# Kernel optimization log

Hardware: AMD Instinct MI355X
Metric: run time of the kernel (lower is better)

## Reference

```python
import jax, jax.numpy as jnp
import numpy as np
from jax import lax

N, D, H, O = 16384, 512, 1024, 512
G, E, K = 3, 4, 2
ALPHA = 0.01


def setup_inputs() -> dict:
    key = jax.random.key(0)
    ks = jax.random.split(key, 16)

    def lin(k, out_d, in_d):
        s = 1.0 / np.sqrt(in_d)
        return jax.random.uniform(k, (out_d, in_d), jnp.float32, -s, s)

    x = jax.random.normal(ks[0], (N, D), jnp.float32)
    Wm = lin(ks[1], G, D)
    bm = jnp.zeros((G,), jnp.float32)
    # group routers stacked: [G, E, D]
    Wr = jax.random.uniform(ks[2], (G, E, D), jnp.float32, -1 / np.sqrt(D), 1 / np.sqrt(D))
    br = jnp.zeros((G, E), jnp.float32)
    # expert params stacked over (group, expert)
    W1 = jax.random.uniform(ks[3], (G, E, H, D), jnp.float32, -1 / np.sqrt(D), 1 / np.sqrt(D))
    b1 = jnp.zeros((G, E, H), jnp.float32)
    W2 = jax.random.uniform(ks[4], (G, E, H, H), jnp.float32, -1 / np.sqrt(H), 1 / np.sqrt(H))
    b2 = jnp.zeros((G, E, H), jnp.float32)
    Wp = jax.random.uniform(ks[5], (G, E, H, D), jnp.float32, -1 / np.sqrt(D), 1 / np.sqrt(D))
    bp = jnp.zeros((G, E, H), jnp.float32)
    W3 = jax.random.uniform(ks[6], (G, E, O, H), jnp.float32, -1 / np.sqrt(H), 1 / np.sqrt(H))
    b3 = jnp.zeros((G, E, O), jnp.float32)
    return {"x": x, "Wm": Wm, "bm": bm, "Wr": Wr, "br": br,
            "W1": W1, "b1": b1, "W2": W2, "b2": b2,
            "Wp": Wp, "bp": bp, "W3": W3, "b3": b3}


def _expert(x, W1, b1, W2, b2, Wp, bp, W3, b3):
    # residual MLP (dropout in eval mode => identity)
    h = jax.nn.relu(x @ W1.T + b1)
    h = h @ W2.T + b2
    ident = x @ Wp.T + bp  # projection (input_dim != hidden_dim)
    h = jax.nn.relu(h + ident)
    return h @ W3.T + b3


def reference(x, Wm, bm, Wr, br, W1, b1, W2, b2, Wp, bp, W3, b3):
    n = x.shape[0]
    # ---- meta (top-1 group) routing ----
    meta_logits = x @ Wm.T + bm                         # [N, G]
    g = jnp.argmax(meta_logits, axis=1)                 # top-1 group per token
    pm = jax.nn.softmax(meta_logits, axis=1).mean(0)    # [G]
    aux = ALPHA * G * jnp.sum(pm * pm)
    # ---- per-group router logits, gathered for each token's group ----
    logits_all = jnp.einsum('nd,ged->nge', x, Wr) + br  # [N, G, E]
    sel = jnp.take_along_axis(logits_all, g[:, None, None], axis=1)[:, 0, :]  # [N, E]
    # ---- group-level load-balancing aux loss (over tokens in each group) ----
    probs = jax.nn.softmax(sel, axis=-1)                # [N, E]
    onehot_g = (g[:, None] == jnp.arange(G)[None, :])   # [N, G] bool
    cnt = onehot_g.sum(0)                               # [G]
    mean_g = (onehot_g.astype(x.dtype).T @ probs) / jnp.maximum(cnt, 1)[:, None].astype(x.dtype)
    aux = aux + jnp.sum(jnp.where(cnt > 0, ALPHA * E * jnp.sum(mean_g * mean_g, -1), 0.0))
    # ---- top-k expert weights within selected group (softmax over the k logits) ----
    vals, idx = lax.top_k(sel, K)                       # [N, K]
    w = jax.nn.softmax(vals, axis=-1)                   # [N, K]
    cw = jnp.zeros((n, E), x.dtype).at[jnp.arange(n)[:, None], idx].set(w)   # [N, E]
    combine = cw[:, None, :] * onehot_g[:, :, None].astype(x.dtype)          # [N, G, E]
    # ---- expert compute + combine (loop over the fixed small set of experts) ----
    out = jnp.zeros((n, O), x.dtype)
    for gi in range(G):
        for e in range(E):
            y = _expert(x, W1[gi, e], b1[gi, e], W2[gi, e], b2[gi, e],
                        Wp[gi, e], bp[gi, e], W3[gi, e], b3[gi, e])
            out = out + combine[:, gi, e:e + 1] * y
    return out, aux
```

## Files before the change

kernel.cpp:

```cpp
#include <hip/hip_runtime.h>
#include <hip/hip_bf16.h>

#define N_TOK 16384
#define DDIM  512
#define HDIM  1024
#define ODIM  512
#define NG    3
#define NE    4
#define NGE   12
#define TASK_CAP 272

typedef __bf16 bf16x8 __attribute__((ext_vector_type(8)));
typedef float  f32x4  __attribute__((ext_vector_type(4)));
typedef unsigned int u32;

__device__ __forceinline__ void gld_lds16(const void* gsrc, void* ldst) {
    __builtin_amdgcn_global_load_lds(
        (const __attribute__((address_space(1))) u32*)gsrc,
        (__attribute__((address_space(3))) u32*)ldst, 16, 0, 0);
}

static constexpr size_t OFF_WSLOT = 512;
static constexpr size_t OFF_ELIST = OFF_WSLOT + (size_t)N_TOK*2*4;
static constexpr size_t OFF_TASK  = 917504;
static constexpr size_t OFF_XBF   = 1048576;
static constexpr size_t OFF_W1    = OFF_XBF + (size_t)N_TOK*DDIM*2;
static constexpr size_t OFF_W2    = OFF_W1  + (size_t)NGE*HDIM*DDIM*2;
static constexpr size_t OFF_WP    = OFF_W2  + (size_t)NGE*HDIM*HDIM*2;
static constexpr size_t OFF_W3    = OFF_WP  + (size_t)NGE*HDIM*DDIM*2;
static constexpr size_t OFF_H1    = OFF_W3  + (size_t)NGE*ODIM*HDIM*2;
static constexpr size_t OFF_U     = OFF_H1  + (size_t)N_TOK*2*HDIM*2;
static constexpr size_t OFF_Y     = OFF_U   + (size_t)N_TOK*2*HDIM*2;
static constexpr size_t WS_NEED   = OFF_Y   + (size_t)N_TOK*2*ODIM*2;

__global__ void cast_all_k(const float* __restrict__ x,  const float* __restrict__ w1,
                           const float* __restrict__ w2, const float* __restrict__ wp,
                           const float* __restrict__ w3,
                           __bf16* xbf, __bf16* w1b, __bf16* w2b, __bf16* wpb, __bf16* w3b) {
    int tid = blockIdx.x * blockDim.x + threadIdx.x;
    int stride = gridDim.x * blockDim.x;
    auto seg = [&](const float* __restrict__ s, __bf16* __restrict__ d, int n4) {
        const float4* s4 = (const float4*)s;
        uint2* d4 = (uint2*)d;
        for (int i = tid; i < n4; i += stride) {
            float4 v = s4[i];
            union { __bf16 h[4]; uint2 u; } o;
            o.h[0] = (__bf16)v.x; o.h[1] = (__bf16)v.y;
            o.h[2] = (__bf16)v.z; o.h[3] = (__bf16)v.w;
            d4[i] = o.u;
        }
    };
    seg(x,  xbf, N_TOK*DDIM/4);
    seg(w1, w1b, NGE*HDIM*DDIM/4);
    seg(w2, w2b, NGE*HDIM*HDIM/4);
    seg(wp, wpb, NGE*HDIM*DDIM/4);
    seg(w3, w3b, NGE*ODIM*HDIM/4);
}

__global__ __launch_bounds__(256) void routing_k(
        const float* __restrict__ x,  const float* __restrict__ Wm,
        const float* __restrict__ bm, const float* __restrict__ Wr,
        const float* __restrict__ br,
        float* pmsum, float* psum, int* cnt, int* ecount,
        int* elist, float* wslot) {
    __shared__ float lpm[NG];
    __shared__ float lpsum[NGE];
    __shared__ int   lcnt[NG];
    __shared__ int   lec[NGE];
    __shared__ int   lbase[NGE];
    __shared__ int   lentry[NGE][64];

    int tid = threadIdx.x;
    if (tid < NG)  { lpm[tid] = 0.f; lcnt[tid] = 0; }
    if (tid < NGE) { lpsum[tid] = 0.f; lec[tid] = 0; }
    __syncthreads();

    int wid = tid >> 6, lane = tid & 63;

    #pragma unroll 1
    for (int i = 0; i < 16; ++i) {
        int t = blockIdx.x * 64 + i * 4 + wid;

        const float4* xr = (const float4*)(x + (size_t)t * DDIM);
        float4 xa = xr[lane*2], xb = xr[lane*2+1];

        float meta[NG];
        #pragma unroll
        for (int gi = 0; gi < NG; ++gi) {
            const float4* w = (const float4*)(Wm + gi*DDIM);
            float4 wa = w[lane*2], wb = w[lane*2+1];
            float s = xa.x*wa.x + xa.y*wa.y + xa.z*wa.z + xa.w*wa.w
                    + xb.x*wb.x + xb.y*wb.y + xb.z*wb.z + xb.w*wb.w;
            #pragma unroll
            for (int off = 32; off > 0; off >>= 1) s += __shfl_xor(s, off);
            meta[gi] = s + bm[gi];
        }
        int g = 0;
        if (meta[1] > meta[g]) g = 1;
        if (meta[2] > meta[g]) g = 2;

        float mm = fmaxf(meta[0], fmaxf(meta[1], meta[2]));
        float e0 = expf(meta[0]-mm), e1 = expf(meta[1]-mm), e2 = expf(meta[2]-mm);
        float inv = 1.f / (e0 + e1 + e2);

        float sel[NE];
        #pragma unroll
        for (int e = 0; e < NE; ++e) {
            const float4* w = (const float4*)(Wr + (size_t)(g*NE + e)*DDIM);
            float4 wa = w[lane*2], wb = w[lane*2+1];
            float s = xa.x*wa.x + xa.y*wa.y + xa.z*wa.z + xa.w*wa.w
                    + xb.x*wb.x + xb.y*wb.y + xb.z*wb.z + xb.w*wb.w;
            #pragma unroll
            for (int off = 32; off > 0; off >>= 1) s += __shfl_xor(s, off);
            sel[e] = s + br[g*NE + e];
        }
        float ms = fmaxf(fmaxf(sel[0],sel[1]), fmaxf(sel[2],sel[3]));
        float pe[NE]; float ss = 0.f;
        #pragma unroll
        for (int e = 0; e < NE; ++e) { pe[e] = expf(sel[e]-ms); ss += pe[e]; }
        float invs = 1.f / ss;

        int i0 = 0;
        #pragma unroll
        for (int e = 1; e < NE; ++e) if (sel[e] > sel[i0]) i0 = e;
        int i1 = (i0 == 0) ? 1 : 0;
        #pragma unroll
        for (int e = 0; e < NE; ++e) if (e != i0 && sel[e] > sel[i1]) i1 = e;
        float ew = expf(sel[i1] - sel[i0]);
        float wden = 1.f / (1.f + ew);

        if (lane == 0) {
            atomicAdd(&lpm[0], e0*inv);
            atomicAdd(&lpm[1], e1*inv);
            atomicAdd(&lpm[2], e2*inv);
            #pragma unroll
            for (int e = 0; e < NE; ++e) atomicAdd(&lpsum[g*NE + e], pe[e]*invs);
            atomicAdd(&lcnt[g], 1);
            int ee0 = g*NE + i0, ee1 = g*NE + i1;
            int p0 = atomicAdd(&lec[ee0], 1);
            lentry[ee0][p0] = t*2;
            int p1 = atomicAdd(&lec[ee1], 1);
            lentry[ee1][p1] = t*2 + 1;
            wslot[t*2]   = wden;
            wslot[t*2+1] = ew * wden;
        }
    }
    __syncthreads();

    if (tid < NG)  { atomicAdd(pmsum + tid, lpm[tid]); atomicAdd(cnt + tid, lcnt[tid]); }
    if (tid < NGE) { atomicAdd(psum + tid, lpsum[tid]);
                     lbase[tid] = atomicAdd(ecount + tid, lec[tid]); }
    __syncthreads();

    for (int e = wid; e < NGE; e += 4) {
        int c = lec[e], base = lbase[e];
        for (int j = lane; j < c; j += 64)
            elist[e*N_TOK + base + j] = lentry[e][j];
    }
}

__global__ void finalize_aux_k(const float* pmsum, const float* psum, const int* cnt,
                               const int* ecount, int2* tasks, int* ntasks,
                               float* outAux) {
    if (threadIdx.x != 0 || blockIdx.x != 0) return;
    float s = 0.f;
    for (int i = 0; i < NG; ++i) { float p = pmsum[i] / (float)N_TOK; s += p*p; }
    float aux = 0.01f * NG * s;
    for (int gg = 0; gg < NG; ++gg) {
        int c = cnt[gg];
        if (c > 0) {
            float s2 = 0.f;
            for (int e = 0; e < NE; ++e) { float m = psum[gg*NE+e] / (float)c; s2 += m*m; }
            aux += 0.01f * NE * s2;
        }
    }
    *outAux = aux;
    int nt = 0;
    for (int ge = 0; ge < NGE; ++ge) {
        int c = ecount[ge];
        for (int m0 = 0; m0 < c; m0 += 128) tasks[nt++] = make_int2(ge, m0);
    }
    *ntasks = nt;
}

template<int NDIM, bool RELU, bool TWOPASS>
__global__ __launch_bounds__(256) void expert_gemm_k(
        const __bf16* __restrict__ A1, int shift1, int k1, const __bf16* __restrict__ B1,
        const __bf16* __restrict__ A2, int shift2, int k2, const __bf16* __restrict__ B2,
        const float* __restrict__ bias1, const float* __restrict__ bias2,
        __bf16* __restrict__ Out,
        const int* __restrict__ ecount, const int* __restrict__ elist,
        const int2* __restrict__ tasks, const int* __restrict__ ntasks) {
    if (blockIdx.y >= *ntasks) return;
    int2 tk = tasks[blockIdx.y];
    int ge = tk.x, m0 = tk.y;
    int cntE = ecount[ge];
    int n0 = blockIdx.x * 128;

    __shared__ __align__(16) char ldsA[2][16384];
    __shared__ __align__(16) char ldsB[2][16384];
    __shared__ int ents[128];

    int tid = threadIdx.x;
    if (tid < 128) {
        int r = m0 + tid;
        if (r >= cntE) r = cntE - 1;
        ents[tid] = elist[ge*N_TOK + r];
    }
    __syncthreads();

    int lane = tid & 63, wv = tid >> 6;
    int wm = wv >> 1, wn = wv & 1;
    int lr = lane & 15, lg = lane >> 4;
    int rl = lane >> 3;
    int csw = (lane & 7) ^ rl;
    int rsw = lr & 7;

    const char* sA1[4]; const char* sB1[4];
    const char* sA2[4]; const char* sB2[4];
    size_t rowB1 = (size_t)k1 * 2;
    const char* Bb1 = (const char*)(B1 + (size_t)ge * NDIM * k1) + (size_t)n0 * rowB1;
    #pragma unroll
    for (int j = 0; j < 4; ++j) {
        int r = wv*32 + j*8 + rl;
        sA1[j] = (const char*)A1 + (size_t)(ents[r] >> shift1) * rowB1 + (size_t)csw*16;
        sB1[j] = Bb1 + (size_t)r * rowB1 + (size_t)csw*16;
    }
    if constexpr (TWOPASS) {
        size_t rowB2 = (size_t)k2 * 2;
        const char* Bb2 = (const char*)(B2 + (size_t)ge * NDIM * k2) + (size_t)n0 * rowB2;
        #pragma unroll
        for (int j = 0; j < 4; ++j) {
            int r = wv*32 + j*8 + rl;
            sA2[j] = (const char*)A2 + (size_t)(ents[r] >> shift2) * rowB2 + (size_t)csw*16;
            sB2[j] = Bb2 + (size_t)r * rowB2 + (size_t)csw*16;
        }
    }

    int nk1 = k1 >> 6;
    int nk  = TWOPASS ? nk1 + (k2 >> 6) : nk1;

    auto stage = [&](int s) {
        int b = s & 1;
        if (!TWOPASS || s < nk1) {
            size_t ko = (size_t)s << 7;
            #pragma unroll
            for (int j = 0; j < 4; ++j) {
                gld_lds16(sA1[j] + ko, ldsA[b] + (wv*4 + j)*1024);
                gld_lds16(sB1[j] + ko, ldsB[b] + (wv*4 + j)*1024);
            }
        } else {
            size_t ko = (size_t)(s - nk1) << 7;
            #pragma unroll
            for (int j = 0; j < 4; ++j) {
                gld_lds16(sA2[j] + ko, ldsA[b] + (wv*4 + j)*1024);
                gld_lds16(sB2[j] + ko, ldsB[b] + (wv*4 + j)*1024);
            }
        }
    };

    f32x4 acc[4][4] = {};

    stage(0);
    __syncthreads();

    #pragma unroll 1
    for (int s = 0; s < nk; ++s) {
        if (s + 1 < nk) stage(s + 1);
        const char* bA = ldsA[s & 1];
        const char* bB = ldsB[s & 1];
        #pragma unroll
        for (int kk = 0; kk < 2; ++kk) {
            bf16x8 av[4], bv[4];
            #pragma unroll
            for (int mi = 0; mi < 4; ++mi) {
                int ar = wm*64 + mi*16 + lr;
                av[mi] = *(const bf16x8*)(bA + ar*128 + ((((kk*4+lg) ^ rsw)) << 4));
            }
            #pragma unroll
            for (int ni = 0; ni < 4; ++ni) {
                int br_ = wn*64 + ni*16 + lr;
                bv[ni] = *(const bf16x8*)(bB + br_*128 + ((((kk*4+lg) ^ rsw)) << 4));
            }
            #pragma unroll
            for (int mi = 0; mi < 4; ++mi)
                #pragma unroll
                for (int ni = 0; ni < 4; ++ni)
                    acc[mi][ni] = __builtin_amdgcn_mfma_f32_16x16x32_bf16(
                        av[mi], bv[ni], acc[mi][ni], 0, 0, 0);
        }
        __syncthreads();
    }

    #pragma unroll
    for (int ni = 0; ni < 4; ++ni) {
        int col = n0 + wn*64 + ni*16 + lr;
        float b = bias1[(size_t)ge*NDIM + col];
        if constexpr (TWOPASS) b += bias2[(size_t)ge*NDIM + col];
        #pragma unroll
        for (int mi = 0; mi < 4; ++mi) {
            #pragma unroll
            for (int j = 0; j < 4; ++j) {
                int rloc = wm*64 + mi*16 + lg*4 + j;
                if (m0 + rloc < cntE) {
                    float v = acc[mi][ni][j] + b;
                    if constexpr (RELU) v = fmaxf(v, 0.f);
                    Out[(size_t)ents[rloc] * NDIM + col] = (__bf16)v;
                }
            }
        }
    }
}

__global__ void combine_k(const __bf16* __restrict__ Y, const float* __restrict__ wslot,
                          float* __restrict__ out) {
    int idx = blockIdx.x * blockDim.x + threadIdx.x;
    int t = idx >> 6;
    int o = (idx & 63) * 8;
    bf16x8 y0 = *(const bf16x8*)(Y + (size_t)(2*t)   * ODIM + o);
    bf16x8 y1 = *(const bf16x8*)(Y + (size_t)(2*t+1) * ODIM + o);
    float w0 = wslot[2*t], w1 = wslot[2*t+1];
    float4 r0, r1;
    r0.x = w0*(float)y0[0] + w1*(float)y1[0];
    r0.y = w0*(float)y0[1] + w1*(float)y1[1];
    r0.z = w0*(float)y0[2] + w1*(float)y1[2];
    r0.w = w0*(float)y0[3] + w1*(float)y1[3];
    r1.x = w0*(float)y0[4] + w1*(float)y1[4];
    r1.y = w0*(float)y0[5] + w1*(float)y1[5];
    r1.z = w0*(float)y0[6] + w1*(float)y1[6];
    r1.w = w0*(float)y0[7] + w1*(float)y1[7];
    float* op = out + (size_t)t * ODIM + o;
    ((float4*)op)[0] = r0;
    ((float4*)op)[1] = r1;
}

extern "C" void kernel_launch(void* const* d_in, const int* in_sizes, int n_in,
                              void* d_out, int out_size, void* d_ws, size_t ws_size,
                              hipStream_t stream) {
    const float* x  = (const float*)d_in[0];
    const float* Wm = (const float*)d_in[1];
    const float* bm = (const float*)d_in[2];
    const float* Wr = (const float*)d_in[3];
    const float* br = (const float*)d_in[4];
    const float* W1 = (const float*)d_in[5];
    const float* b1 = (const float*)d_in[6];
    const float* W2 = (const float*)d_in[7];
    const float* b2 = (const float*)d_in[8];
    const float* Wp = (const float*)d_in[9];
    const float* bp = (const float*)d_in[10];
    const float* W3 = (const float*)d_in[11];
    const float* b3 = (const float*)d_in[12];

    if (ws_size < WS_NEED) return;

    char* ws = (char*)d_ws;
    float* outp = (float*)d_out;

    float* pmsum  = (float*)ws;
    float* psum   = (float*)ws + 4;
    int*   cnt    = (int*)ws + 16;
    int*   ecount = (int*)ws + 20;
    int*   ntasks = (int*)ws + 34;
    float* wslot  = (float*)(ws + OFF_WSLOT);
    int*   elist  = (int*)(ws + OFF_ELIST);
    int2*  tasks  = (int2*)(ws + OFF_TASK);
    __bf16* xbf = (__bf16*)(ws + OFF_XBF);
    __bf16* w1b = (__bf16*)(ws + OFF_W1);
    __bf16* w2b = (__bf16*)(ws + OFF_W2);
    __bf16* wpb = (__bf16*)(ws + OFF_WP);
    __bf16* w3b = (__bf16*)(ws + OFF_W3);
    __bf16* H1  = (__bf16*)(ws + OFF_H1);
    __bf16* U   = (__bf16*)(ws + OFF_U);
    __bf16* Y   = (__bf16*)(ws + OFF_Y);

    hipMemsetAsync(d_ws, 0, 512, stream);

    cast_all_k<<<4096, 256, 0, stream>>>(x, W1, W2, Wp, W3, xbf, w1b, w2b, wpb, w3b);

    routing_k<<<256, 256, 0, stream>>>(x, Wm, bm, Wr, br,
                                       pmsum, psum, cnt, ecount, elist, wslot);

    finalize_aux_k<<<1, 64, 0, stream>>>(pmsum, psum, cnt, ecount, tasks, ntasks,
                                         outp + (size_t)N_TOK*ODIM);

    dim3 gA(HDIM/128, TASK_CAP, 1);
    expert_gemm_k<HDIM, true, false><<<gA, 256, 0, stream>>>(
        xbf, 1, DDIM, w1b, nullptr, 0, 0, nullptr, b1, nullptr, H1,
        ecount, elist, tasks, ntasks);

    expert_gemm_k<HDIM, true, true><<<gA, 256, 0, stream>>>(
        H1, 0, HDIM, w2b, xbf, 1, DDIM, wpb, b2, bp, U,
        ecount, elist, tasks, ntasks);

    dim3 gC(ODIM/128, TASK_CAP, 1);
    expert_gemm_k<ODIM, false, false><<<gC, 256, 0, stream>>>(
        U, 0, HDIM, w3b, nullptr, 0, 0, nullptr, b3, nullptr, Y,
        ecount, elist, tasks, ntasks);

    combine_k<<<4096, 256, 0, stream>>>(Y, wslot, outp);
}
```

Baseline: 473.9 us.

## Fuse three expert GEMMs into one kernel keeping hidden activations in LDS

Replaces the three separate grouped expert GEMM launches with one fused kernel. Each 512-thread block processes a 64-token tile through W1, W2+Wp and W3, keeping the hidden activations in a 128KB LDS buffer instead of writing H1 and U to global memory. Tasks are remapped so consecutive tasks land on the same XCD. The cost is that weight operands are now read straight from global memory with no LDS staging or double buffering, occupancy is limited by the large LDS footprint, and only 64-row tiles with one block per tile are available for parallelism.

Result: slower. 736.2 us (+55.3%).

```diff
diff --git a/kernel.cpp b/kernel.cpp
--- a/kernel.cpp
+++ b/kernel.cpp
@@ -8,17 +8,10 @@
 #define NG    3
 #define NE    4
 #define NGE   12
-#define TASK_CAP 272
+#define TASK_CAP 544
 
 typedef __bf16 bf16x8 __attribute__((ext_vector_type(8)));
 typedef float  f32x4  __attribute__((ext_vector_type(4)));
-typedef unsigned int u32;
-
-__device__ __forceinline__ void gld_lds16(const void* gsrc, void* ldst) {
-    __builtin_amdgcn_global_load_lds(
-        (const __attribute__((address_space(1))) u32*)gsrc,
-        (__attribute__((address_space(3))) u32*)ldst, 16, 0, 0);
-}
 
 static constexpr size_t OFF_WSLOT = 512;
 static constexpr size_t OFF_ELIST = OFF_WSLOT + (size_t)N_TOK*2*4;
@@ -28,9 +21,7 @@
 static constexpr size_t OFF_W2    = OFF_W1  + (size_t)NGE*HDIM*DDIM*2;
 static constexpr size_t OFF_WP    = OFF_W2  + (size_t)NGE*HDIM*HDIM*2;
 static constexpr size_t OFF_W3    = OFF_WP  + (size_t)NGE*HDIM*DDIM*2;
-static constexpr size_t OFF_H1    = OFF_W3  + (size_t)NGE*ODIM*HDIM*2;
-static constexpr size_t OFF_U     = OFF_H1  + (size_t)N_TOK*2*HDIM*2;
-static constexpr size_t OFF_Y     = OFF_U   + (size_t)N_TOK*2*HDIM*2;
+static constexpr size_t OFF_Y     = OFF_W3  + (size_t)NGE*ODIM*HDIM*2;
 static constexpr size_t WS_NEED   = OFF_Y   + (size_t)N_TOK*2*ODIM*2;
 
 __global__ void cast_all_k(const float* __restrict__ x,  const float* __restrict__ w1,
@@ -178,137 +169,197 @@
     int nt = 0;
     for (int ge = 0; ge < NGE; ++ge) {
         int c = ecount[ge];
-        for (int m0 = 0; m0 < c; m0 += 128) tasks[nt++] = make_int2(ge, m0);
+        for (int m0 = 0; m0 < c; m0 += 64) tasks[nt++] = make_int2(ge, m0);
     }
     *ntasks = nt;
 }
 
-template<int NDIM, bool RELU, bool TWOPASS>
-__global__ __launch_bounds__(256) void expert_gemm_k(
-        const __bf16* __restrict__ A1, int shift1, int k1, const __bf16* __restrict__ B1,
-        const __bf16* __restrict__ A2, int shift2, int k2, const __bf16* __restrict__ B2,
-        const float* __restrict__ bias1, const float* __restrict__ bias2,
-        __bf16* __restrict__ Out,
+__global__ __launch_bounds__(512, 2) void fused_expert_k(
+        const __bf16* __restrict__ xbf,
+        const __bf16* __restrict__ w1b, const __bf16* __restrict__ w2b,
+        const __bf16* __restrict__ wpb, const __bf16* __restrict__ w3b,
+        const float* __restrict__ b1, const float* __restrict__ b2,
+        const float* __restrict__ bp, const float* __restrict__ b3,
+        __bf16* __restrict__ Y,
         const int* __restrict__ ecount, const int* __restrict__ elist,
         const int2* __restrict__ tasks, const int* __restrict__ ntasks) {
-    if (blockIdx.y >= *ntasks) return;
-    int2 tk = tasks[blockIdx.y];
+    __shared__ __align__(16) char hbuf[64 * 2048];
+    __shared__ int ents[64];
+
+    int T = *ntasks;
+    int q = T >> 3, r = T & 7;
+    int xcd = blockIdx.x & 7, idx = blockIdx.x >> 3;
+    int pc = (xcd < r) ? q + 1 : q;
+    if (idx >= pc) return;
+    int task = ((xcd < r) ? xcd * (q + 1) : r * (q + 1) + (xcd - r) * q) + idx;
+    int2 tk = tasks[task];
     int ge = tk.x, m0 = tk.y;
     int cntE = ecount[ge];
-    int n0 = blockIdx.x * 128;
-
-    __shared__ __align__(16) char ldsA[2][16384];
-    __shared__ __align__(16) char ldsB[2][16384];
-    __shared__ int ents[128];
 
     int tid = threadIdx.x;
-    if (tid < 128) {
-        int r = m0 + tid;
-        if (r >= cntE) r = cntE - 1;
-        ents[tid] = elist[ge*N_TOK + r];
+    if (tid < 64) {
+        int rr = m0 + tid;
+        if (rr >= cntE) rr = cntE - 1;
+        ents[tid] = elist[ge*N_TOK + rr];
     }
     __syncthreads();
 
     int lane = tid & 63, wv = tid >> 6;
-    int wm = wv >> 1, wn = wv & 1;
     int lr = lane & 15, lg = lane >> 4;
-    int rl = lane >> 3;
-    int csw = (lane & 7) ^ rl;
-    int rsw = lr & 7;
-
-    const char* sA1[4]; const char* sB1[4];
-    const char* sA2[4]; const char* sB2[4];
-    size_t rowB1 = (size_t)k1 * 2;
-    const char* Bb1 = (const char*)(B1 + (size_t)ge * NDIM * k1) + (size_t)n0 * rowB1;
-    #pragma unroll
-    for (int j = 0; j < 4; ++j) {
-        int r = wv*32 + j*8 + rl;
-        sA1[j] = (const char*)A1 + (size_t)(ents[r] >> shift1) * rowB1 + (size_t)csw*16;
-        sB1[j] = Bb1 + (size_t)r * rowB1 + (size_t)csw*16;
-    }
-    if constexpr (TWOPASS) {
-        size_t rowB2 = (size_t)k2 * 2;
-        const char* Bb2 = (const char*)(B2 + (size_t)ge * NDIM * k2) + (size_t)n0 * rowB2;
-        #pragma unroll
-        for (int j = 0; j < 4; ++j) {
-            int r = wv*32 + j*8 + rl;
-            sA2[j] = (const char*)A2 + (size_t)(ents[r] >> shift2) * rowB2 + (size_t)csw*16;
-            sB2[j] = Bb2 + (size_t)r * rowB2 + (size_t)csw*16;
-        }
-    }
-
-    int nk1 = k1 >> 6;
-    int nk  = TWOPASS ? nk1 + (k2 >> 6) : nk1;
-
-    auto stage = [&](int s) {
-        int b = s & 1;
-        if (!TWOPASS || s < nk1) {
-            size_t ko = (size_t)s << 7;
+
+    const char* px[4];
+    #pragma unroll
+    for (int mi = 0; mi < 4; ++mi)
+        px[mi] = (const char*)xbf + (size_t)(ents[mi*16 + lr] >> 1) * (DDIM*2) + lg*16;
+
+    auto lds_at = [&](int row, int g) -> char* {
+        return hbuf + row*2048 + (((g ^ (row & 7)) << 4));
+    };
+
+    f32x4 acc[4][8];
+
+    #pragma unroll
+    for (int mi = 0; mi < 4; ++mi)
+        #pragma unroll
+        for (int ni = 0; ni < 8; ++ni) acc[mi][ni] = (f32x4){0.f,0.f,0.f,0.f};
+    {
+        const char* pb[8];
+        #pragma unroll
+        for (int ni = 0; ni < 8; ++ni)
+            pb[ni] = (const char*)w1b + ((size_t)ge*HDIM + wv*128 + ni*16 + lr) * (DDIM*2) + lg*16;
+        #pragma unroll 2
+        for (int k0 = 0; k0 < DDIM; k0 += 32) {
+            bf16x8 av[4], bv[8];
+            #pragma unroll
+            for (int mi = 0; mi < 4; ++mi) av[mi] = *(const bf16x8*)(px[mi] + k0*2);
+            #pragma unroll
+            for (int ni = 0; ni < 8; ++ni) bv[ni] = *(const bf16x8*)(pb[ni] + k0*2);
+            #pragma unroll
+            for (int mi = 0; mi < 4; ++mi)
+                #pragma unroll
+                for (int ni = 0; ni < 8; ++ni)
+                    acc[mi][ni] = __builtin_amdgcn_mfma_f32_16x16x32_bf16(
+                        av[mi], bv[ni], acc[mi][ni], 0, 0, 0);
+        }
+    }
+    #pragma unroll
+    for (int ni = 0; ni < 8; ++ni) {
+        int col = wv*128 + ni*16 + lr;
+        float bb = b1[(size_t)ge*HDIM + col];
+        int g = col >> 3, cb = (col & 7) * 2;
+        #pragma unroll
+        for (int mi = 0; mi < 4; ++mi)
             #pragma unroll
             for (int j = 0; j < 4; ++j) {
-                gld_lds16(sA1[j] + ko, ldsA[b] + (wv*4 + j)*1024);
-                gld_lds16(sB1[j] + ko, ldsB[b] + (wv*4 + j)*1024);
+                int row = mi*16 + lg*4 + j;
+                float v = fmaxf(acc[mi][ni][j] + bb, 0.f);
+                *(__bf16*)(hbuf + row*2048 + (((g ^ (row & 7)) << 4) | cb)) = (__bf16)v;
             }
-        } else {
-            size_t ko = (size_t)(s - nk1) << 7;
+    }
+    __syncthreads();
+
+    #pragma unroll
+    for (int mi = 0; mi < 4; ++mi)
+        #pragma unroll
+        for (int ni = 0; ni < 8; ++ni) acc[mi][ni] = (f32x4){0.f,0.f,0.f,0.f};
+    {
+        const char* pb[8];
+        #pragma unroll
+        for (int ni = 0; ni < 8; ++ni)
+            pb[ni] = (const char*)w2b + ((size_t)ge*HDIM + wv*128 + ni*16 + lr) * (HDIM*2) + lg*16;
+        #pragma unroll 2
+        for (int k0 = 0; k0 < HDIM; k0 += 32) {
+            bf16x8 av[4], bv[8];
+            #pragma unroll
+            for (int mi = 0; mi < 4; ++mi) {
+                int row = mi*16 + lr;
+                av[mi] = *(const bf16x8*)lds_at(row, (k0 >> 3) + lg);
+            }
+            #pragma unroll
+            for (int ni = 0; ni < 8; ++ni) bv[ni] = *(const bf16x8*)(pb[ni] + k0*2);
+            #pragma unroll
+            for (int mi = 0; mi < 4; ++mi)
+                #pragma unroll
+                for (int ni = 0; ni < 8; ++ni)
+                    acc[mi][ni] = __builtin_amdgcn_mfma_f32_16x16x32_bf16(
+                        av[mi], bv[ni], acc[mi][ni], 0, 0, 0);
+        }
+        const char* pw[8];
+        #pragma unroll
+        for (int ni = 0; ni < 8; ++ni)
+            pw[ni] = (const char*)wpb + ((size_t)ge*HDIM + wv*128 + ni*16 + lr) * (DDIM*2) + lg*16;
+        #pragma unroll 2
+        for (int k0 = 0; k0 < DDIM; k0 += 32) {
+            bf16x8 av[4], bv[8];
+            #pragma unroll
+            for (int mi = 0; mi < 4; ++mi) av[mi] = *(const bf16x8*)(px[mi] + k0*2);
+            #pragma unroll
+            for (int ni = 0; ni < 8; ++ni) bv[ni] = *(const bf16x8*)(pw[ni] + k0*2);
+            #pragma unroll
+            for (int mi = 0; mi < 4; ++mi)
+                #pragma unroll
+                for (int ni = 0; ni < 8; ++ni)
+                    acc[mi][ni] = __builtin_amdgcn_mfma_f32_16x16x32_bf16(
+                        av[mi], bv[ni], acc[mi][ni], 0, 0, 0);
+        }
+    }
+    __syncthreads();
+    #pragma unroll
+    for (int ni = 0; ni < 8; ++ni) {
+        int col = wv*128 + ni*16 + lr;
+        float bb = b2[(size_t)ge*HDIM + col] + bp[(size_t)ge*HDIM + col];
+        int g = col >> 3, cb = (col & 7) * 2;
+        #pragma unroll
+        for (int mi = 0; mi < 4; ++mi)
             #pragma unroll
             for (int j = 0; j < 4; ++j) {
-                gld_lds16(sA2[j] + ko, ldsA[b] + (wv*4 + j)*1024);
-                gld_lds16(sB2[j] + ko, ldsB[b] + (wv*4 + j)*1024);
+                int row = mi*16 + lg*4 + j;
+                float v = fmaxf(acc[mi][ni][j] + bb, 0.f);
+                *(__bf16*)(hbuf + row*2048 + (((g ^ (row & 7)) << 4) | cb)) = (__bf16)v;
             }
-        }
-    };
-
-    f32x4 acc[4][4] = {};
-
-    stage(0);
-    __syncthreads();
-
-    #pragma unroll 1
-    for (int s = 0; s < nk; ++s) {
-        if (s + 1 < nk) stage(s + 1);
-        const char* bA = ldsA[s & 1];
-        const char* bB = ldsB[s & 1];
-        #pragma unroll
-        for (int kk = 0; kk < 2; ++kk) {
+    }
+    __syncthreads();
+
+    f32x4 acc3[4][4];
+    #pragma unroll
+    for (int mi = 0; mi < 4; ++mi)
+        #pragma unroll
+        for (int ni = 0; ni < 4; ++ni) acc3[mi][ni] = (f32x4){0.f,0.f,0.f,0.f};
+    {
+        const char* pb[4];
+        #pragma unroll
+        for (int ni = 0; ni < 4; ++ni)
+            pb[ni] = (const char*)w3b + ((size_t)ge*ODIM + wv*64 + ni*16 + lr) * (HDIM*2) + lg*16;
+        #pragma unroll 2
+        for (int k0 = 0; k0 < HDIM; k0 += 32) {
             bf16x8 av[4], bv[4];
             #pragma unroll
             for (int mi = 0; mi < 4; ++mi) {
-                int ar = wm*64 + mi*16 + lr;
-                av[mi] = *(const bf16x8*)(bA + ar*128 + ((((kk*4+lg) ^ rsw)) << 4));
+                int row = mi*16 + lr;
+                av[mi] = *(const bf16x8*)lds_at(row, (k0 >> 3) + lg);
             }
             #pragma unroll
-            for (int ni = 0; ni < 4; ++ni) {
-                int br_ = wn*64 + ni*16 + lr;
-                bv[ni] = *(const bf16x8*)(bB + br_*128 + ((((kk*4+lg) ^ rsw)) << 4));
-            }
+            for (int ni = 0; ni < 4; ++ni) bv[ni] = *(const bf16x8*)(pb[ni] + k0*2);
             #pragma unroll
             for (int mi = 0; mi < 4; ++mi)
                 #pragma unroll
                 for (int ni = 0; ni < 4; ++ni)
-                    acc[mi][ni] = __builtin_amdgcn_mfma_f32_16x16x32_bf16(
-                        av[mi], bv[ni], acc[mi][ni], 0, 0, 0);
-        }
-        __syncthreads();
-    }
-
+                    acc3[mi][ni] = __builtin_amdgcn_mfma_f32_16x16x32_bf16(
+                        av[mi], bv[ni], acc3[mi][ni], 0, 0, 0);
+        }
+    }
     #pragma unroll
     for (int ni = 0; ni < 4; ++ni) {
-        int col = n0 + wn*64 + ni*16 + lr;
-        float b = bias1[(size_t)ge*NDIM + col];
-        if constexpr (TWOPASS) b += bias2[(size_t)ge*NDIM + col];
-        #pragma unroll
-        for (int mi = 0; mi < 4; ++mi) {
+        int col = wv*64 + ni*16 + lr;
+        float bb = b3[(size_t)ge*ODIM + col];
+        #pragma unroll
+        for (int mi = 0; mi < 4; ++mi)
             #pragma unroll
             for (int j = 0; j < 4; ++j) {
-                int rloc = wm*64 + mi*16 + lg*4 + j;
-                if (m0 + rloc < cntE) {
-                    float v = acc[mi][ni][j] + b;
-                    if constexpr (RELU) v = fmaxf(v, 0.f);
-                    Out[(size_t)ents[rloc] * NDIM + col] = (__bf16)v;
-                }
+                int rloc = mi*16 + lg*4 + j;
+                if (m0 + rloc < cntE)
+                    Y[(size_t)ents[rloc] * ODIM + col] = (__bf16)(acc3[mi][ni][j] + bb);
             }
-        }
     }
 }
 
@@ -369,8 +420,6 @@
     __bf16* w2b = (__bf16*)(ws + OFF_W2);
     __bf16* wpb = (__bf16*)(ws + OFF_WP);
     __bf16* w3b = (__bf16*)(ws + OFF_W3);
-    __bf16* H1  = (__bf16*)(ws + OFF_H1);
-    __bf16* U   = (__bf16*)(ws + OFF_U);
     __bf16* Y   = (__bf16*)(ws + OFF_Y);
 
     hipMemsetAsync(d_ws, 0, 512, stream);
@@ -383,19 +432,9 @@
     finalize_aux_k<<<1, 64, 0, stream>>>(pmsum, psum, cnt, ecount, tasks, ntasks,
                                          outp + (size_t)N_TOK*ODIM);
 
-    dim3 gA(HDIM/128, TASK_CAP, 1);
-    expert_gemm_k<HDIM, true, false><<<gA, 256, 0, stream>>>(
-        xbf, 1, DDIM, w1b, nullptr, 0, 0, nullptr, b1, nullptr, H1,
+    fused_expert_k<<<TASK_CAP, 512, 0, stream>>>(
+        xbf, w1b, w2b, wpb, w3b, b1, b2, bp, b3, Y,
         ecount, elist, tasks, ntasks);
 
-    expert_gemm_k<HDIM, true, true><<<gA, 256, 0, stream>>>(
-        H1, 0, HDIM, w2b, xbf, 1, DDIM, wpb, b2, bp, U,
-        ecount, elist, tasks, ntasks);
-
-    dim3 gC(ODIM/128, TASK_CAP, 1);
-    expert_gemm_k<ODIM, false, false><<<gC, 256, 0, stream>>>(
-        U, 0, HDIM, w3b, nullptr, 0, 0, nullptr, b3, nullptr, Y,
-        ecount, elist, tasks, ntasks);
-
     combine_k<<<4096, 256, 0, stream>>>(Y, wslot, outp);
 }
```
